# Optimization experiments

Measured on AMD Instinct MI355X. Metric: run time of the kernel, lower is better.

## Reference

```python
import jax, jax.numpy as jnp
import numpy as np

B, S, D, H = 2, 2048, 1024, 16
HD = D // H
NEG = -10000000000.0

def setup_inputs() -> dict:
    key = jax.random.key(0)
    ks = jax.random.split(key, 9)
    s = 1.0 / np.sqrt(D)
    return {
        "x": jax.random.normal(ks[0], (B, S, D), dtype=jnp.float32),
        "Wq": jax.random.uniform(ks[1], (D, D), jnp.float32, -s, s),
        "bq": jax.random.uniform(ks[2], (D,), jnp.float32, -s, s),
        "Wk": jax.random.uniform(ks[3], (D, D), jnp.float32, -s, s),
        "bk": jax.random.uniform(ks[4], (D,), jnp.float32, -s, s),
        "Wv": jax.random.uniform(ks[5], (D, D), jnp.float32, -s, s),
        "bv": jax.random.uniform(ks[6], (D,), jnp.float32, -s, s),
        "Wo": jax.random.uniform(ks[7], (D, D), jnp.float32, -s, s),
        "bo": jax.random.uniform(ks[8], (D,), jnp.float32, -s, s),
    }

def reference(x, Wq, bq, Wk, bk, Wv, bv, Wo, bo):
    b, s, _ = x.shape
    def split_heads(t):
        return t.reshape(b, s, H, HD).transpose(0, 2, 1, 3)  # [b,h,s,hd]
    Q = split_heads(x @ Wq + bq)
    K = split_heads(x @ Wk + bk)
    V = split_heads(x @ Wv + bv)
    scores = jnp.einsum('bhqd,bhkd->bhqk', Q, K) / jnp.sqrt(jnp.float32(HD))
    causal = jnp.tril(jnp.ones((s, s), dtype=bool))
    scores = jnp.where(causal[None, None], scores, NEG)
    attn = jax.nn.softmax(scores, axis=-1)
    ctx = jnp.einsum('bhqk,bhkd->bhqd', attn, V)
    ctx = ctx.transpose(0, 2, 1, 3).reshape(b, s, D)
    return ctx @ Wo + bo
```

## Files before the change

kernel.cpp:

```cpp
#include <hip/hip_runtime.h>
#include <hip/hip_bf16.h>

#define BB 2
#define SS 2048
#define DD 1024
#define HH 16
#define HD 64
#define MM (BB*SS)

typedef __attribute__((ext_vector_type(8))) short bf16x8;
typedef __attribute__((ext_vector_type(4))) float f32x4;
typedef __attribute__((ext_vector_type(16))) float f32x16;

#define QSCALE 0.18033688f

static __device__ __forceinline__ unsigned short f2bf(float f) {
    unsigned int u = __builtin_bit_cast(unsigned int, f);
    u += 0x7fffu + ((u >> 16) & 1u);
    return (unsigned short)(u >> 16);
}

static __device__ __forceinline__ void gload16(const unsigned short* g, unsigned short* l) {
    __builtin_amdgcn_global_load_lds(
        (const __attribute__((address_space(1))) unsigned int*)g,
        (__attribute__((address_space(3))) unsigned int*)l, 16, 0, 0);
}

__global__ __launch_bounds__(256) void prep_kernel(const float* __restrict__ x,
                                                   const float* __restrict__ W0,
                                                   const float* __restrict__ W1,
                                                   const float* __restrict__ W2,
                                                   const float* __restrict__ W3,
                                                   unsigned short* __restrict__ xb,
                                                   unsigned short* __restrict__ Wt)
{
    const int t = threadIdx.x;
    const int bid = blockIdx.x;
    if (bid < 2048) {
        const size_t i = ((size_t)bid * 256 + t) * 8;
        float4 a = *(const float4*)(x + i);
        float4 b = *(const float4*)(x + i + 4);
        union { unsigned short u[8]; bf16x8 v; } pk;
        pk.u[0] = f2bf(a.x); pk.u[1] = f2bf(a.y); pk.u[2] = f2bf(a.z); pk.u[3] = f2bf(a.w);
        pk.u[4] = f2bf(b.x); pk.u[5] = f2bf(b.y); pk.u[6] = f2bf(b.z); pk.u[7] = f2bf(b.w);
        *(bf16x8*)(xb + i) = pk.v;
        return;
    }
    __shared__ unsigned short Ts[64][72];
    const int wsel = (bid - 2048) >> 8;
    const int rem  = (bid - 2048) & 255;
    const float* W = wsel == 0 ? W0 : wsel == 1 ? W1 : wsel == 2 ? W2 : W3;
    unsigned short* out = Wt + (size_t)wsel * DD * DD;
    const int n0 = (rem & 15) * 64, k0 = (rem >> 4) * 64;
#pragma unroll
    for (int i = 0; i < 4; ++i) {
        const int r = (t >> 4) + i * 16;
        const int c = (t & 15) * 4;
        float4 v = *(const float4*)(W + (size_t)(k0 + r) * DD + n0 + c);
        Ts[c + 0][r] = f2bf(v.x); Ts[c + 1][r] = f2bf(v.y);
        Ts[c + 2][r] = f2bf(v.z); Ts[c + 3][r] = f2bf(v.w);
    }
    __syncthreads();
#pragma unroll
    for (int j = 0; j < 2; ++j) {
        const int ch = j * 256 + t;
        const int rn = ch >> 3, ck = (ch & 7) * 8;
        bf16x8 v = *(const bf16x8*)&Ts[rn][ck];
        *(bf16x8*)(out + (size_t)(n0 + rn) * DD + k0 + ck) = v;
    }
}

__global__ __launch_bounds__(256) void gemm_mfma(const unsigned short* __restrict__ A,
                                                 const unsigned short* __restrict__ Bt,
                                                 const float* __restrict__ bias0,
                                                 const float* __restrict__ bias1,
                                                 const float* __restrict__ bias2,
                                                 unsigned short* __restrict__ Qb,
                                                 unsigned short* __restrict__ Kb,
                                                 unsigned short* __restrict__ Vb,
                                                 float* __restrict__ outf,
                                                 int mode)
{
    __shared__ unsigned short As[2][128 * 64];
    __shared__ unsigned short Bs[2][128 * 64];

    const int t = threadIdx.x;
    const int w = t >> 6, l = t & 63;
    const int lane16 = l & 15, quad = l >> 4;
    const int m0 = blockIdx.x * 128, n0 = blockIdx.y * 128;
    const int wm = (w & 1) * 64, wn = (w >> 1) * 64;

    f32x4 acc[4][4] = {};

    int srow[4], skcg[4];
#pragma unroll
    for (int j = 0; j < 4; ++j) {
        const int c = t + j * 256;
        srow[j] = c >> 3;
        skcg[j] = (c & 7) ^ (srow[j] & 7);
    }

#pragma unroll
    for (int j = 0; j < 4; ++j) {
        const int c = t + j * 256;
        gload16(A  + (size_t)(m0 + srow[j]) * DD + skcg[j] * 8, &As[0][c * 8]);
        gload16(Bt + (size_t)(n0 + srow[j]) * DD + skcg[j] * 8, &Bs[0][c * 8]);
    }
    __syncthreads();

#pragma unroll 2
    for (int kt = 0; kt < 16; ++kt) {
        const int cur = kt & 1;
        if (kt + 1 < 16) {
            const int k1 = (kt + 1) * 64;
#pragma unroll
            for (int j = 0; j < 4; ++j) {
                const int c = t + j * 256;
                gload16(A  + (size_t)(m0 + srow[j]) * DD + k1 + skcg[j] * 8, &As[cur ^ 1][c * 8]);
                gload16(Bt + (size_t)(n0 + srow[j]) * DD + k1 + skcg[j] * 8, &Bs[cur ^ 1][c * 8]);
            }
        }
#pragma unroll
        for (int h = 0; h < 2; ++h) {
            bf16x8 af[4], bfr[4];
#pragma unroll
            for (int mt = 0; mt < 4; ++mt) {
                const int row = wm + mt * 16 + lane16;
                af[mt] = *(const bf16x8*)&As[cur][(row * 8 + ((h * 4 + quad) ^ (row & 7))) * 8];
            }
#pragma unroll
            for (int nt = 0; nt < 4; ++nt) {
                const int row = wn + nt * 16 + lane16;
                bfr[nt] = *(const bf16x8*)&Bs[cur][(row * 8 + ((h * 4 + quad) ^ (row & 7))) * 8];
            }
#pragma unroll
            for (int mt = 0; mt < 4; ++mt)
#pragma unroll
                for (int nt = 0; nt < 4; ++nt)
                    acc[mt][nt] = __builtin_amdgcn_mfma_f32_16x16x32_bf16(af[mt], bfr[nt], acc[mt][nt], 0, 0, 0);
        }
        __syncthreads();
    }

    if (mode == 0) {
        const int which = n0 >> 10;
        const float* bias = which == 0 ? bias0 : which == 1 ? bias1 : bias2;
#pragma unroll
        for (int nt = 0; nt < 4; ++nt) {
            const int gcol = n0 + wn + nt * 16 + lane16;
            const int cd = gcol & 1023;
            const float bv = bias[cd];
            const int h_ = cd >> 6, d = cd & 63;
            if (which == 2) {
#pragma unroll
                for (int mt = 0; mt < 4; ++mt) {
                    const int row0 = m0 + wm + mt * 16 + quad * 4;
                    const int b_ = row0 >> 11, s0 = row0 & 2047;
                    union { unsigned short u[4]; uint2 v; } pk;
#pragma unroll
                    for (int r = 0; r < 4; ++r) pk.u[r] = f2bf(acc[mt][nt][r] + bv);
                    *(uint2*)(Vb + ((size_t)(b_ * HH + h_) * HD + d) * SS + s0) = pk.v;
                }
            } else {
                unsigned short* dst3 = which == 0 ? Qb : Kb;
                const float sc_ = which == 0 ? QSCALE : 1.0f;
#pragma unroll
                for (int mt = 0; mt < 4; ++mt)
#pragma unroll
                    for (int r = 0; r < 4; ++r) {
                        const int row = m0 + wm + mt * 16 + quad * 4 + r;
                        const int b_ = row >> 11, s_ = row & 2047;
                        dst3[(((size_t)(b_ * HH + h_) * SS + s_) * HD) + d] =
                            f2bf((acc[mt][nt][r] + bv) * sc_);
                    }
            }
        }
    } else {
#pragma unroll
        for (int nt = 0; nt < 4; ++nt) {
            const int gcol = n0 + wn + nt * 16 + lane16;
            const float bv = bias0[gcol];
#pragma unroll
            for (int mt = 0; mt < 4; ++mt)
#pragma unroll
                for (int r = 0; r < 4; ++r) {
                    const int row = m0 + wm + mt * 16 + quad * 4 + r;
                    outf[(size_t)row * DD + gcol] = acc[mt][nt][r] + bv;
                }
        }
    }
}

__global__ __launch_bounds__(512) void attn_mfma(const unsigned short* __restrict__ Q,
                                                 const unsigned short* __restrict__ K,
                                                 const unsigned short* __restrict__ V,
                                                 unsigned short* __restrict__ ctx)
{
    __shared__ unsigned short Ks[4][4096];
    __shared__ unsigned short Vs[4][4096];

    const int t = threadIdx.x;
    const int w = t >> 6, l = t & 63;
    const int l31 = l & 31, hi = l >> 5;
    const int qg = w & 3, par = w >> 2;
    const int bid = blockIdx.x;
    const int halfg = bid >> 8, idx = bid & 255;
    const int qb_ = idx >> 5;
    const int qblk = halfg ? qb_ : 15 - qb_;
    const int hb = idx & 31;
    const int h = hb & 15, b = hb >> 4;
    const int q0 = qblk * 128;
    const size_t bh = (size_t)(b * HH + h) * SS;
    const unsigned short* Vg = V + (size_t)(b * HH + h) * HD * SS;

    const int wq0 = q0 + qg * 32;
    bf16x8 qf[4];
#pragma unroll
    for (int dt = 0; dt < 4; ++dt)
        qf[dt] = *(const bf16x8*)(Q + (bh + wq0 + l31) * HD + dt * 16 + hi * 8);

    f32x16 ot[2] = {};
    float lp = 0.f;

    const int ntiles = 2 * qblk + 2;
    const int sr = t >> 3;
    const int sg = (t & 7) ^ (sr & 7);

    {
        gload16(K  + (bh + sr) * HD + sg * 8,            &Ks[0][t * 8]);
        gload16(K  + (bh + 64 + sr) * HD + sg * 8,       &Ks[1][t * 8]);
        gload16(Vg + (size_t)sr * SS + sg * 8,           &Vs[0][t * 8]);
        gload16(Vg + (size_t)sr * SS + 64 + sg * 8,      &Vs[1][t * 8]);
    }
    __syncthreads();

    const int nsup = ntiles >> 1;
    for (int st = 0; st < nsup; ++st) {
        if (2 * st + 2 < ntiles) {
            const int ka = (2 * st + 2) * 64, kb = ka + 64;
            const int ba = (2 * st + 2) & 3, bb2 = (2 * st + 3) & 3;
            gload16(K  + (bh + ka + sr) * HD + sg * 8,       &Ks[ba][t * 8]);
            gload16(K  + (bh + kb + sr) * HD + sg * 8,       &Ks[bb2][t * 8]);
            gload16(Vg + (size_t)sr * SS + ka + sg * 8,      &Vs[ba][t * 8]);
            gload16(Vg + (size_t)sr * SS + kb + sg * 8,      &Vs[bb2][t * 8]);
        }

        const int mt = 2 * st + par;
        const int k0 = mt * 64;
        if (k0 <= wq0 + 31) {
            const unsigned short* Kt = Ks[mt & 3];
            const unsigned short* Vt = Vs[mt & 3];

            f32x16 s[2] = {};
            __builtin_amdgcn_s_setprio(1);
#pragma unroll
            for (int dt = 0; dt < 4; ++dt) {
#pragma unroll
                for (int kh = 0; kh < 2; ++kh) {
                    const int row = kh * 32 + l31;
                    bf16x8 kf = *(const bf16x8*)&Kt[(row * 8 + ((dt * 2 + hi) ^ (row & 7))) * 8];
                    s[kh] = __builtin_amdgcn_mfma_f32_32x32x16_bf16(kf, qf[dt], s[kh], 0, 0, 0);
                }
            }
            __builtin_amdgcn_s_setprio(0);

            if (k0 + 63 > wq0) {
                const int q = wq0 + l31;
#pragma unroll
                for (int kh = 0; kh < 2; ++kh)
#pragma unroll
                    for (int r = 0; r < 16; ++r) {
                        const int k = k0 + kh * 32 + (r & 3) + 8 * (r >> 2) + 4 * hi;
                        if (k > q) s[kh][r] = -1e30f;
                    }
            }

#pragma unroll
            for (int kh = 0; kh < 2; ++kh) {
#pragma unroll
                for (int r = 0; r < 16; ++r) s[kh][r] = __builtin_amdgcn_exp2f(s[kh][r]);
                const float t0 = (s[kh][0] + s[kh][1]) + (s[kh][2] + s[kh][3]);
                const float t1 = (s[kh][4] + s[kh][5]) + (s[kh][6] + s[kh][7]);
                const float t2 = (s[kh][8] + s[kh][9]) + (s[kh][10] + s[kh][11]);
                const float t3 = (s[kh][12] + s[kh][13]) + (s[kh][14] + s[kh][15]);
                lp += (t0 + t1) + (t2 + t3);
            }

#pragma unroll
            for (int kh = 0; kh < 2; ++kh) {
#pragma unroll
                for (int c = 0; c < 2; ++c) {
                    const int rb = c * 8;
                    unsigned int w0, w1, w2, w3;
                    asm("v_cvt_pk_bf16_f32 %0, %1, %2" : "=v"(w0) : "v"(s[kh][rb + 0]), "v"(s[kh][rb + 1]));
                    asm("v_cvt_pk_bf16_f32 %0, %1, %2" : "=v"(w2) : "v"(s[kh][rb + 4]), "v"(s[kh][rb + 5]));
                    asm("v_cvt_pk_bf16_f32 %0, %1, %2" : "=v"(w1) : "v"(s[kh][rb + 2]), "v"(s[kh][rb + 3]));
                    asm("v_cvt_pk_bf16_f32 %0, %1, %2" : "=v"(w3) : "v"(s[kh][rb + 6]), "v"(s[kh][rb + 7]));
                    asm("v_permlane32_swap_b32 %0, %1" : "+v"(w0), "+v"(w2));
                    asm("v_permlane32_swap_b32 %0, %1" : "+v"(w1), "+v"(w3));
                    union { unsigned int u[4]; bf16x8 v; } pa;
                    pa.u[0] = w0; pa.u[1] = w1; pa.u[2] = w2; pa.u[3] = w3;
                    const int chunk = kh * 4 + c * 2 + hi;
                    const int rlo = l31, rhi2 = 32 + l31;
                    bf16x8 v0 = *(const bf16x8*)&Vt[(rlo * 8 + (chunk ^ (rlo & 7))) * 8];
                    bf16x8 v1 = *(const bf16x8*)&Vt[(rhi2 * 8 + (chunk ^ (rhi2 & 7))) * 8];
                    __builtin_amdgcn_s_setprio(1);
                    ot[0] = __builtin_amdgcn_mfma_f32_32x32x16_bf16(v0, pa.v, ot[0], 0, 0, 0);
                    ot[1] = __builtin_amdgcn_mfma_f32_32x32x16_bf16(v1, pa.v, ot[1], 0, 0, 0);
                    __builtin_amdgcn_s_setprio(0);
                }
            }
        }
        __syncthreads();
    }

    float* Osh = (float*)&Ks[0][0];
    float* Lsh = (float*)&Vs[0][0];
    if (par == 1) {
        float* o = Osh + qg * 2048;
#pragma unroll
        for (int a2 = 0; a2 < 2; ++a2)
#pragma unroll
            for (int r = 0; r < 16; ++r) o[(a2 * 16 + r) * 64 + l] = ot[a2][r];
        Lsh[qg * 64 + l] = lp;
    }
    __syncthreads();
    if (par == 0) {
        float* o = Osh + qg * 2048;
#pragma unroll
        for (int a2 = 0; a2 < 2; ++a2)
#pragma unroll
            for (int r = 0; r < 16; ++r) ot[a2][r] += o[(a2 * 16 + r) * 64 + l];
        lp += Lsh[qg * 64 + l];

        lp += __shfl_xor(lp, 32);
        const float inv = 1.f / lp;

        const int qrow = wq0 + l31;
        unsigned short* dst = ctx + ((size_t)(b * SS) + qrow) * DD + h * HD;
#pragma unroll
        for (int a2 = 0; a2 < 2; ++a2)
#pragma unroll
            for (int u = 0; u < 4; ++u) {
                const int d0 = a2 * 32 + 8 * u + 4 * hi;
                union { unsigned short u4[4]; uint2 v; } pk;
#pragma unroll
                for (int r = 0; r < 4; ++r) pk.u4[r] = f2bf(ot[a2][4 * u + r] * inv);
                *(uint2*)(dst + d0) = pk.v;
            }
    }
}

extern "C" void kernel_launch(void* const* d_in, const int* in_sizes, int n_in,
                              void* d_out, int out_size, void* d_ws, size_t ws_size,
                              hipStream_t stream) {
    const float* x  = (const float*)d_in[0];
    const float* Wq = (const float*)d_in[1];
    const float* bq = (const float*)d_in[2];
    const float* Wk = (const float*)d_in[3];
    const float* bk = (const float*)d_in[4];
    const float* Wv = (const float*)d_in[5];
    const float* bv = (const float*)d_in[6];
    const float* Wo = (const float*)d_in[7];
    const float* bo = (const float*)d_in[8];
    float* out = (float*)d_out;

    unsigned short* xb  = (unsigned short*)d_ws;
    unsigned short* Wt  = xb  + (size_t)MM * DD;
    unsigned short* Qb  = Wt  + (size_t)4 * DD * DD;
    unsigned short* Kb  = Qb  + (size_t)MM * DD;
    unsigned short* Vb  = Kb  + (size_t)MM * DD;
    unsigned short* ctxb = Vb + (size_t)MM * DD;

    prep_kernel<<<2048 + 1024, 256, 0, stream>>>(x, Wq, Wk, Wv, Wo, xb, Wt);

    gemm_mfma<<<dim3(MM / 128, 3072 / 128), 256, 0, stream>>>(
        xb, Wt, bq, bk, bv, Qb, Kb, Vb, nullptr, 0);

    attn_mfma<<<(SS / 128) * HH * BB, 512, 0, stream>>>(Qb, Kb, Vb, ctxb);

    gemm_mfma<<<dim3(MM / 128, DD / 128), 256, 0, stream>>>(
        ctxb, Wt + (size_t)3 * DD * DD, bo, nullptr, nullptr,
        nullptr, nullptr, nullptr, out, 1);
}
```

Measured before the change: 183.5 us.

## Read K and V directly from global memory in attention, drop LDS staging

Removes the four-buffer LDS staging of K/V tiles, the async global-to-LDS loads and the per-iteration block barrier. Each wave now loops only over its own causal tiles and loads K and V fragments straight from global memory, relying on L1/L2 caches for reuse across the eight waves. This eliminates barrier stalls and the imbalance across wave parities, but it loses the prefetch overlap and shared reuse, and V reads become strided across rows.

```diff
diff --git a/kernel.cpp b/kernel.cpp
--- a/kernel.cpp
+++ b/kernel.cpp
@@ -196,8 +196,8 @@
                                                  const unsigned short* __restrict__ V,
                                                  unsigned short* __restrict__ ctx)
 {
-    __shared__ unsigned short Ks[4][4096];
-    __shared__ unsigned short Vs[4][4096];
+    __shared__ float Osh[4][32][64];
+    __shared__ float Lsh[4][64];
 
     const int t = threadIdx.x;
     const int w = t >> 6, l = t & 63;
@@ -222,116 +222,85 @@
     f32x16 ot[2] = {};
     float lp = 0.f;
 
-    const int ntiles = 2 * qblk + 2;
-    const int sr = t >> 3;
-    const int sg = (t & 7) ^ (sr & 7);
-
-    {
-        gload16(K  + (bh + sr) * HD + sg * 8,            &Ks[0][t * 8]);
-        gload16(K  + (bh + 64 + sr) * HD + sg * 8,       &Ks[1][t * 8]);
-        gload16(Vg + (size_t)sr * SS + sg * 8,           &Vs[0][t * 8]);
-        gload16(Vg + (size_t)sr * SS + 64 + sg * 8,      &Vs[1][t * 8]);
-    }
-    __syncthreads();
-
-    const int nsup = ntiles >> 1;
-    for (int st = 0; st < nsup; ++st) {
-        if (2 * st + 2 < ntiles) {
-            const int ka = (2 * st + 2) * 64, kb = ka + 64;
-            const int ba = (2 * st + 2) & 3, bb2 = (2 * st + 3) & 3;
-            gload16(K  + (bh + ka + sr) * HD + sg * 8,       &Ks[ba][t * 8]);
-            gload16(K  + (bh + kb + sr) * HD + sg * 8,       &Ks[bb2][t * 8]);
-            gload16(Vg + (size_t)sr * SS + ka + sg * 8,      &Vs[ba][t * 8]);
-            gload16(Vg + (size_t)sr * SS + kb + sg * 8,      &Vs[bb2][t * 8]);
-        }
-
-        const int mt = 2 * st + par;
+    const int lastT = (wq0 + 31) >> 6;
+
+    for (int mt = par; mt <= lastT; mt += 2) {
         const int k0 = mt * 64;
-        if (k0 <= wq0 + 31) {
-            const unsigned short* Kt = Ks[mt & 3];
-            const unsigned short* Vt = Vs[mt & 3];
-
-            f32x16 s[2] = {};
-            __builtin_amdgcn_s_setprio(1);
-#pragma unroll
-            for (int dt = 0; dt < 4; ++dt) {
-#pragma unroll
-                for (int kh = 0; kh < 2; ++kh) {
-                    const int row = kh * 32 + l31;
-                    bf16x8 kf = *(const bf16x8*)&Kt[(row * 8 + ((dt * 2 + hi) ^ (row & 7))) * 8];
-                    s[kh] = __builtin_amdgcn_mfma_f32_32x32x16_bf16(kf, qf[dt], s[kh], 0, 0, 0);
+
+        f32x16 s[2] = {};
+        __builtin_amdgcn_s_setprio(1);
+#pragma unroll
+        for (int dt = 0; dt < 4; ++dt) {
+#pragma unroll
+            for (int kh = 0; kh < 2; ++kh) {
+                const int row = k0 + kh * 32 + l31;
+                bf16x8 kf = *(const bf16x8*)(K + (bh + row) * HD + dt * 16 + hi * 8);
+                s[kh] = __builtin_amdgcn_mfma_f32_32x32x16_bf16(kf, qf[dt], s[kh], 0, 0, 0);
+            }
+        }
+        __builtin_amdgcn_s_setprio(0);
+
+        if (k0 + 63 > wq0) {
+            const int q = wq0 + l31;
+#pragma unroll
+            for (int kh = 0; kh < 2; ++kh)
+#pragma unroll
+                for (int r = 0; r < 16; ++r) {
+                    const int k = k0 + kh * 32 + (r & 3) + 8 * (r >> 2) + 4 * hi;
+                    if (k > q) s[kh][r] = -1e30f;
                 }
-            }
-            __builtin_amdgcn_s_setprio(0);
-
-            if (k0 + 63 > wq0) {
-                const int q = wq0 + l31;
-#pragma unroll
-                for (int kh = 0; kh < 2; ++kh)
-#pragma unroll
-                    for (int r = 0; r < 16; ++r) {
-                        const int k = k0 + kh * 32 + (r & 3) + 8 * (r >> 2) + 4 * hi;
-                        if (k > q) s[kh][r] = -1e30f;
-                    }
-            }
-
-#pragma unroll
-            for (int kh = 0; kh < 2; ++kh) {
-#pragma unroll
-                for (int r = 0; r < 16; ++r) s[kh][r] = __builtin_amdgcn_exp2f(s[kh][r]);
-                const float t0 = (s[kh][0] + s[kh][1]) + (s[kh][2] + s[kh][3]);
-                const float t1 = (s[kh][4] + s[kh][5]) + (s[kh][6] + s[kh][7]);
-                const float t2 = (s[kh][8] + s[kh][9]) + (s[kh][10] + s[kh][11]);
-                const float t3 = (s[kh][12] + s[kh][13]) + (s[kh][14] + s[kh][15]);
-                lp += (t0 + t1) + (t2 + t3);
-            }
-
-#pragma unroll
-            for (int kh = 0; kh < 2; ++kh) {
-#pragma unroll
-                for (int c = 0; c < 2; ++c) {
-                    const int rb = c * 8;
-                    unsigned int w0, w1, w2, w3;
-                    asm("v_cvt_pk_bf16_f32 %0, %1, %2" : "=v"(w0) : "v"(s[kh][rb + 0]), "v"(s[kh][rb + 1]));
-                    asm("v_cvt_pk_bf16_f32 %0, %1, %2" : "=v"(w2) : "v"(s[kh][rb + 4]), "v"(s[kh][rb + 5]));
-                    asm("v_cvt_pk_bf16_f32 %0, %1, %2" : "=v"(w1) : "v"(s[kh][rb + 2]), "v"(s[kh][rb + 3]));
-                    asm("v_cvt_pk_bf16_f32 %0, %1, %2" : "=v"(w3) : "v"(s[kh][rb + 6]), "v"(s[kh][rb + 7]));
-                    asm("v_permlane32_swap_b32 %0, %1" : "+v"(w0), "+v"(w2));
-                    asm("v_permlane32_swap_b32 %0, %1" : "+v"(w1), "+v"(w3));
-                    union { unsigned int u[4]; bf16x8 v; } pa;
-                    pa.u[0] = w0; pa.u[1] = w1; pa.u[2] = w2; pa.u[3] = w3;
-                    const int chunk = kh * 4 + c * 2 + hi;
-                    const int rlo = l31, rhi2 = 32 + l31;
-                    bf16x8 v0 = *(const bf16x8*)&Vt[(rlo * 8 + (chunk ^ (rlo & 7))) * 8];
-                    bf16x8 v1 = *(const bf16x8*)&Vt[(rhi2 * 8 + (chunk ^ (rhi2 & 7))) * 8];
-                    __builtin_amdgcn_s_setprio(1);
-                    ot[0] = __builtin_amdgcn_mfma_f32_32x32x16_bf16(v0, pa.v, ot[0], 0, 0, 0);
-                    ot[1] = __builtin_amdgcn_mfma_f32_32x32x16_bf16(v1, pa.v, ot[1], 0, 0, 0);
-                    __builtin_amdgcn_s_setprio(0);
-                }
-            }
-        }
-        __syncthreads();
-    }
-
-    float* Osh = (float*)&Ks[0][0];
-    float* Lsh = (float*)&Vs[0][0];
+        }
+
+#pragma unroll
+        for (int kh = 0; kh < 2; ++kh) {
+#pragma unroll
+            for (int r = 0; r < 16; ++r) s[kh][r] = __builtin_amdgcn_exp2f(s[kh][r]);
+            const float t0 = (s[kh][0] + s[kh][1]) + (s[kh][2] + s[kh][3]);
+            const float t1 = (s[kh][4] + s[kh][5]) + (s[kh][6] + s[kh][7]);
+            const float t2 = (s[kh][8] + s[kh][9]) + (s[kh][10] + s[kh][11]);
+            const float t3 = (s[kh][12] + s[kh][13]) + (s[kh][14] + s[kh][15]);
+            lp += (t0 + t1) + (t2 + t3);
+        }
+
+#pragma unroll
+        for (int kh = 0; kh < 2; ++kh) {
+#pragma unroll
+            for (int c = 0; c < 2; ++c) {
+                const int rb = c * 8;
+                unsigned int w0, w1, w2, w3;
+                asm("v_cvt_pk_bf16_f32 %0, %1, %2" : "=v"(w0) : "v"(s[kh][rb + 0]), "v"(s[kh][rb + 1]));
+                asm("v_cvt_pk_bf16_f32 %0, %1, %2" : "=v"(w2) : "v"(s[kh][rb + 4]), "v"(s[kh][rb + 5]));
+                asm("v_cvt_pk_bf16_f32 %0, %1, %2" : "=v"(w1) : "v"(s[kh][rb + 2]), "v"(s[kh][rb + 3]));
+                asm("v_cvt_pk_bf16_f32 %0, %1, %2" : "=v"(w3) : "v"(s[kh][rb + 6]), "v"(s[kh][rb + 7]));
+                asm("v_permlane32_swap_b32 %0, %1" : "+v"(w0), "+v"(w2));
+                asm("v_permlane32_swap_b32 %0, %1" : "+v"(w1), "+v"(w3));
+                union { unsigned int u[4]; bf16x8 v; } pa;
+                pa.u[0] = w0; pa.u[1] = w1; pa.u[2] = w2; pa.u[3] = w3;
+                const int kc = k0 + (kh * 4 + c * 2 + hi) * 8;
+                bf16x8 v0 = *(const bf16x8*)(Vg + (size_t)l31 * SS + kc);
+                bf16x8 v1 = *(const bf16x8*)(Vg + (size_t)(32 + l31) * SS + kc);
+                __builtin_amdgcn_s_setprio(1);
+                ot[0] = __builtin_amdgcn_mfma_f32_32x32x16_bf16(v0, pa.v, ot[0], 0, 0, 0);
+                ot[1] = __builtin_amdgcn_mfma_f32_32x32x16_bf16(v1, pa.v, ot[1], 0, 0, 0);
+                __builtin_amdgcn_s_setprio(0);
+            }
+        }
+    }
+
     if (par == 1) {
-        float* o = Osh + qg * 2048;
 #pragma unroll
         for (int a2 = 0; a2 < 2; ++a2)
 #pragma unroll
-            for (int r = 0; r < 16; ++r) o[(a2 * 16 + r) * 64 + l] = ot[a2][r];
-        Lsh[qg * 64 + l] = lp;
+            for (int r = 0; r < 16; ++r) Osh[qg][a2 * 16 + r][l] = ot[a2][r];
+        Lsh[qg][l] = lp;
     }
     __syncthreads();
     if (par == 0) {
-        float* o = Osh + qg * 2048;
 #pragma unroll
         for (int a2 = 0; a2 < 2; ++a2)
 #pragma unroll
-            for (int r = 0; r < 16; ++r) ot[a2][r] += o[(a2 * 16 + r) * 64 + l];
-        lp += Lsh[qg * 64 + l];
+            for (int r = 0; r < 16; ++r) ot[a2][r] += Osh[qg][a2 * 16 + r][l];
+        lp += Lsh[qg][l];
 
         lp += __shfl_xor(lp, 32);
         const float inv = 1.f / lp;
```

After: 215.7 us. 1.18x slower.
